# Kernel tuning notes

Measured on AMD Instinct MI355X. Metric: run time of the kernel, lower is better.

## Reference

```python
import jax, jax.numpy as jnp
import numpy as np

SEQ, B, IN, H, GATES = 2048, 64, 64, 128, 4 * 128


def setup_inputs() -> dict:
    key = jax.random.key(0)
    ks = jax.random.split(key, 12)
    s_in = 1.0 / np.sqrt(H)
    return {
        "data": jax.random.normal(ks[0], (SEQ, B, IN), dtype=jnp.float32),
        "Wih0": jax.random.normal(ks[1], (GATES, IN), dtype=jnp.float32) * s_in,
        "Whh0": jax.random.normal(ks[2], (GATES, H), dtype=jnp.float32) * s_in,
        "bih0": jax.random.normal(ks[3], (GATES,), dtype=jnp.float32) * s_in,
        "bhh0": jax.random.normal(ks[4], (GATES,), dtype=jnp.float32) * s_in,
        "Wih1": jax.random.normal(ks[5], (GATES, H), dtype=jnp.float32) * s_in,
        "Whh1": jax.random.normal(ks[6], (GATES, H), dtype=jnp.float32) * s_in,
        "bih1": jax.random.normal(ks[7], (GATES,), dtype=jnp.float32) * s_in,
        "bhh1": jax.random.normal(ks[8], (GATES,), dtype=jnp.float32) * s_in,
        "Wlin": jax.random.normal(ks[9], (1, H), dtype=jnp.float32) * s_in,
        "blin": jax.random.normal(ks[10], (1,), dtype=jnp.float32) * s_in,
    }


def _lstm_layer(x, Wih, Whh, bih, bhh):
    # x: [T, B, D_in]; torch gate order: i, f, g, o
    Bsz = x.shape[1]
    Hd = Whh.shape[1]
    b = bih + bhh
    # Precompute input projections for all timesteps in one big GEMM: [T, B, 4H]
    xproj = jnp.einsum('tbd,gd->tbg', x, Wih) + b

    def step(carry, xp_t):
        h, c = carry
        gates = xp_t + h @ Whh.T  # [B, 4H]
        i, f, g, o = jnp.split(gates, 4, axis=-1)
        i = jax.nn.sigmoid(i)
        f = jax.nn.sigmoid(f)
        g = jnp.tanh(g)
        o = jax.nn.sigmoid(o)
        c = f * c + i * g
        h = o * jnp.tanh(c)
        return (h, c), h

    h0 = jnp.zeros((Bsz, Hd), x.dtype)
    (_, _), ys = jax.lax.scan(step, (h0, h0), xproj)
    return ys  # [T, B, H]


def reference(data, Wih0, Whh0, bih0, bhh0, Wih1, Whh1, bih1, bhh1, Wlin, blin):
    h = _lstm_layer(data, Wih0, Whh0, bih0, bhh0)
    h = _lstm_layer(h, Wih1, Whh1, bih1, bhh1)
    vecs = h @ Wlin.T + blin  # [T, B, 1]
    # NOTE: original module computes tanh(vecs) but returns the pre-tanh vecs.
    return vecs
```

## Files before the change

kernel.cpp:

```cpp
#include <hip/hip_runtime.h>

#define SEQ_T 2048
#define BATCH 64

typedef _Float16 half2v __attribute__((ext_vector_type(2)));
typedef float floatx2 __attribute__((ext_vector_type(2)));

#if defined(__has_builtin)
#  if __has_builtin(__builtin_amdgcn_fdot2)
#    define HAVE_FDOT2 1
#  endif
#endif

__device__ __forceinline__ float fdot2f(half2v a, half2v b, float c) {
#ifdef HAVE_FDOT2
  return __builtin_amdgcn_fdot2(a, b, c, false);
#else
  return c + (float)a[0] * (float)b[0] + (float)a[1] * (float)b[1];
#endif
}

__device__ __forceinline__ floatx2 fma2(floatx2 a, floatx2 b, floatx2 c) {
#if __has_builtin(__builtin_elementwise_fma)
  return __builtin_elementwise_fma(a, b, c);
#else
  floatx2 r;
  r.x = __builtin_fmaf(a.x, b.x, c.x);
  r.y = __builtin_fmaf(a.y, b.y, c.y);
  return r;
#endif
}

__device__ __forceinline__ unsigned int h2u(half2v v) { return __builtin_bit_cast(unsigned int, v); }
__device__ __forceinline__ half2v u2h(unsigned int u) { return __builtin_bit_cast(half2v, u); }

template <int K, bool IN_F32>
__global__ __launch_bounds__(512) void xproj_gemm(
    const void* __restrict__ Xv,
    const float* __restrict__ W,
    const float* __restrict__ bih, const float* __restrict__ bhh,
    unsigned short* __restrict__ xp)
{
  constexpr int MT = 64;
  const int g = threadIdx.x;
  const size_t m0 = (size_t)blockIdx.x * MT;

  __shared__ __align__(16) _Float16 xs[MT * K];

  if constexpr (IN_F32) {
    constexpr int PER = MT * K / 512;
    const float* Xf = (const float*)Xv + m0 * K + (size_t)g * PER;
    _Float16* dst = xs + g * PER;
#pragma unroll
    for (int i = 0; i < PER; i += 4) {
      float4 v = *reinterpret_cast<const float4*>(Xf + i);
      half2v h01; h01[0] = (_Float16)v.x; h01[1] = (_Float16)v.y;
      half2v h23; h23[0] = (_Float16)v.z; h23[1] = (_Float16)v.w;
      uint2 u; u.x = h2u(h01); u.y = h2u(h23);
      *reinterpret_cast<uint2*>(dst + i) = u;
    }
  } else {
    constexpr int PER = MT * K / 512;
    const unsigned short* Xh = (const unsigned short*)Xv + m0 * K + (size_t)g * PER;
#pragma unroll
    for (int i = 0; i < PER / 8; i++)
      reinterpret_cast<uint4*>(xs + g * PER)[i] = reinterpret_cast<const uint4*>(Xh)[i];
  }

  half2v wr[K / 2];
  {
    const float2* p = reinterpret_cast<const float2*>(W + (size_t)g * K);
#pragma unroll
    for (int k = 0; k < K / 2; k++) {
      float2 f = p[k];
      half2v v; v[0] = (_Float16)f.x; v[1] = (_Float16)f.y;
      wr[k] = v;
    }
  }
  const float bias = bih[g] + bhh[g];
  const int out_off = (g & 127) * 4 + (g >> 7);
  __syncthreads();

#pragma unroll 1
  for (int tb = 0; tb < MT; tb++) {
    const uint4* xv = reinterpret_cast<const uint4*>(xs + tb * K);
    float a0 = bias, a1 = 0.f, a2 = 0.f, a3 = 0.f;
#pragma unroll
    for (int i = 0; i < K / 8; i++) {
      const uint4 u = xv[i];
      a0 = fdot2f(wr[4 * i + 0], u2h(u.x), a0);
      a1 = fdot2f(wr[4 * i + 1], u2h(u.y), a1);
      a2 = fdot2f(wr[4 * i + 2], u2h(u.z), a2);
      a3 = fdot2f(wr[4 * i + 3], u2h(u.w), a3);
    }
    const float s = (a0 + a1) + (a2 + a3);
    xp[(m0 + tb) * 512 + out_off] = __builtin_bit_cast(unsigned short, (_Float16)s);
  }
}

struct StepCtx {
  int ks, r, hidx;
  int li0, li1, li2, li3;
  float sc, am, ab;
  bool writer;
};

__device__ __forceinline__ float sigmoid_fast(float x) {
  return 1.f / (1.f + __expf(-x));
}

__device__ __forceinline__ void lstm_step(
    int cur, const StepCtx& cx,
    const floatx2 (&wh)[4][16], float (&hbuf)[2][144],
    unsigned short& pf, const unsigned short*& pf_ptr,
    float& c, unsigned short*& hout_ptr)
{
  const float xpv = (float)__builtin_bit_cast(_Float16, pf);
  pf = *pf_ptr;
  pf_ptr += 2 * BATCH * 512;

  floatx2 a0 = {0.f, 0.f}, a1 = {0.f, 0.f}, a2 = {0.f, 0.f}, a3 = {0.f, 0.f};
  const float4* hv = reinterpret_cast<const float4*>(&hbuf[cur][cx.ks * 36]);
#pragma unroll
  for (int i = 0; i < 8; i++) {
    const float4 u = hv[i];
    floatx2 lo; lo.x = u.x; lo.y = u.y;
    floatx2 hi; hi.x = u.z; hi.y = u.w;
    a0 = fma2(wh[0][2 * i], lo, a0); a0 = fma2(wh[0][2 * i + 1], hi, a0);
    a1 = fma2(wh[1][2 * i], lo, a1); a1 = fma2(wh[1][2 * i + 1], hi, a1);
    a2 = fma2(wh[2][2 * i], lo, a2); a2 = fma2(wh[2][2 * i + 1], hi, a2);
    a3 = fma2(wh[3][2 * i], lo, a3); a3 = fma2(wh[3][2 * i + 1], hi, a3);
  }
  float b0v = a0.x + a0.y;
  float b1v = a1.x + a1.y;
  float b2v = a2.x + a2.y;
  float b3v = a3.x + a3.y;

  const bool q0 = (cx.ks & 1) != 0, q1 = (cx.ks & 2) != 0;
  float s0 = q0 ? b0v : b1v;
  float s1 = q0 ? b2v : b3v;
  float r0 = __shfl_xor(s0, 1);
  float r1 = __shfl_xor(s1, 1);
  float kA = (q0 ? b1v : b0v) + r0;
  float kB = (q0 ? b3v : b2v) + r1;
  float s2 = q1 ? kA : kB;
  float r2 = __shfl_xor(s2, 2);
  float sum = (q1 ? kB : kA) + r2 + xpv;

  float y = cx.am * sigmoid_fast(cx.sc * sum) + cx.ab;

  float gi = __shfl(y, cx.li0);
  float gf = __shfl(y, cx.li1);
  float gg = __shfl(y, cx.li2);
  float go = __shfl(y, cx.li3);

  c = gf * c + gi * gg;
  float th = 2.f * sigmoid_fast(2.f * c) - 1.f;
  float h = go * th;

  if (cx.writer) {
    hbuf[cur ^ 1][cx.hidx] = h;
    *hout_ptr = __builtin_bit_cast(unsigned short, (_Float16)h);
  }
  hout_ptr += BATCH * 128;

  __syncthreads();
}

__global__ __launch_bounds__(512, 2) void lstm_rec2(
    const float* __restrict__ Whh,
    const unsigned short* __restrict__ xp,
    unsigned short* __restrict__ hout)
{
  const int b = blockIdx.x;
  const int tid = threadIdx.x;
  const int l = tid & 63;
  const int w = tid >> 6;
  const int rr = l >> 2;
  const int ks = l & 3;
  const int r = w * 16 + rr;

  __shared__ __align__(16) float hbuf[2][144];

  floatx2 wh[4][16];
#pragma unroll
  for (int g = 0; g < 4; g++) {
    const float4* p = reinterpret_cast<const float4*>(
        Whh + ((size_t)(g * 128 + r)) * 128 + ks * 32);
#pragma unroll
    for (int k = 0; k < 8; k++) {
      float4 f = p[k];
      floatx2 lo; lo.x = f.x; lo.y = f.y;
      floatx2 hi; hi.x = f.z; hi.y = f.w;
      wh[g][2 * k] = lo;
      wh[g][2 * k + 1] = hi;
    }
  }

  StepCtx cx;
  cx.ks = ks; cx.r = r;
  cx.hidx = (r >> 5) * 36 + (r & 31);
  const int lb = l & ~3;
  cx.li0 = lb + 0; cx.li1 = lb + 1; cx.li2 = lb + 2; cx.li3 = lb + 3;
  cx.sc = (ks == 2) ? 2.f : 1.f;
  cx.am = (ks == 2) ? 2.f : 1.f;
  cx.ab = (ks == 2) ? -1.f : 0.f;
  cx.writer = (ks == 0);

  if (tid < 144) { hbuf[0][tid] = 0.f; }

  const unsigned short* xpb = xp + (size_t)b * 512 + tid;
  unsigned short pfa = xpb[0];
  unsigned short pfb = xpb[(size_t)1 * (BATCH * 512)];
  const unsigned short* pA = xpb + (size_t)2 * (BATCH * 512);
  const unsigned short* pB = xpb + (size_t)3 * (BATCH * 512);
  unsigned short* houtp = hout + (size_t)b * 128 + r;
  float c = 0.f;
  __syncthreads();

#pragma unroll 1
  for (int t = 0; t < SEQ_T; t += 2) {
    lstm_step(0, cx, wh, hbuf, pfa, pA, c, houtp);
    lstm_step(1, cx, wh, hbuf, pfb, pB, c, houtp);
  }
}

__global__ __launch_bounds__(256) void final_lin(
    const unsigned short* __restrict__ h1,
    const float* __restrict__ Wlin, const float* __restrict__ blin,
    float* __restrict__ out)
{
  const size_t tb = (size_t)blockIdx.x * 256 + threadIdx.x;
  half2v wl[64];
  const float2* p = reinterpret_cast<const float2*>(Wlin);
#pragma unroll
  for (int k = 0; k < 64; k++) {
    float2 f = p[k];
    half2v v; v[0] = (_Float16)f.x; v[1] = (_Float16)f.y;
    wl[k] = v;
  }
  const uint4* hv = reinterpret_cast<const uint4*>(h1 + tb * 128);
  float a0 = 0.f, a1 = 0.f, a2 = 0.f, a3 = 0.f;
#pragma unroll
  for (int i = 0; i < 16; i++) {
    const uint4 u = hv[i];
    a0 = fdot2f(wl[4 * i + 0], u2h(u.x), a0);
    a1 = fdot2f(wl[4 * i + 1], u2h(u.y), a1);
    a2 = fdot2f(wl[4 * i + 2], u2h(u.z), a2);
    a3 = fdot2f(wl[4 * i + 3], u2h(u.w), a3);
  }
  out[tb] = (a0 + a1) + (a2 + a3) + blin[0];
}

extern "C" void kernel_launch(void* const* d_in, const int* in_sizes, int n_in,
                              void* d_out, int out_size, void* d_ws, size_t ws_size,
                              hipStream_t stream) {
  (void)in_sizes; (void)n_in; (void)out_size; (void)ws_size;

  const float* data = (const float*)d_in[0];
  const float* Wih0 = (const float*)d_in[1];
  const float* Whh0 = (const float*)d_in[2];
  const float* bih0 = (const float*)d_in[3];
  const float* bhh0 = (const float*)d_in[4];
  const float* Wih1 = (const float*)d_in[5];
  const float* Whh1 = (const float*)d_in[6];
  const float* bih1 = (const float*)d_in[7];
  const float* bhh1 = (const float*)d_in[8];
  const float* Wlin = (const float*)d_in[9];
  const float* blin = (const float*)d_in[10];

  unsigned char* ws = (unsigned char*)d_ws;
  unsigned short* xpb = (unsigned short*)ws;
  unsigned short* h0 = (unsigned short*)(ws + (size_t)128 * 1024 * 1024);
  unsigned short* h1 = (unsigned short*)(ws + (size_t)160 * 1024 * 1024);

  const int M = SEQ_T * BATCH;
  const int gemm_blocks = M / 64;

  xproj_gemm<64, true><<<dim3(gemm_blocks), dim3(512), 0, stream>>>(
      data, Wih0, bih0, bhh0, xpb);
  lstm_rec2<<<dim3(BATCH), dim3(512), 0, stream>>>(Whh0, xpb, h0);
  xproj_gemm<128, false><<<dim3(gemm_blocks), dim3(512), 0, stream>>>(
      h0, Wih1, bih1, bhh1, xpb);
  lstm_rec2<<<dim3(BATCH), dim3(512), 0, stream>>>(Whh1, xpb, h1);
  final_lin<<<dim3(M / 256), dim3(256), 0, stream>>>(h1, Wlin, blin, (float*)d_out);
}
```

Before: 3.195 ms.

## Split recurrent LSTM step over 1024 threads with DPP quad reductions

Moves the recurrent kernel from 512 threads, each reducing a 32-element K slice, to 1024 threads that each reduce a 16-element slice. This halves the serial dot-product work per thread on every step. Cross-lane shuffles (ds_bpermute) for the partial-sum reduction and gate broadcast are replaced with DPP quad permutes plus a half-row mirror, which should lower latency on the step's critical path. The cost is a 1024-thread barrier each step and twice as many redundant lanes computing gate activations.

```diff
diff --git a/kernel.cpp b/kernel.cpp
--- a/kernel.cpp
+++ b/kernel.cpp
@@ -33,6 +33,20 @@
 
 __device__ __forceinline__ unsigned int h2u(half2v v) { return __builtin_bit_cast(unsigned int, v); }
 __device__ __forceinline__ half2v u2h(unsigned int u) { return __builtin_bit_cast(half2v, u); }
+
+template <int CTRL>
+__device__ __forceinline__ float qperm(float x) {
+  int xi = __builtin_bit_cast(int, x);
+  int ri = __builtin_amdgcn_update_dpp(xi, xi, CTRL, 0xF, 0xF, true);
+  return __builtin_bit_cast(float, ri);
+}
+#define QP_XOR1   0xB1
+#define QP_XOR2   0x4E
+#define QP_B0     0x00
+#define QP_B1     0x55
+#define QP_B2     0xAA
+#define QP_B3     0xFF
+#define QP_HMIRR  0x141
 
 template <int K, bool IN_F32>
 __global__ __launch_bounds__(512) void xproj_gemm(
@@ -99,10 +113,9 @@
 }
 
 struct StepCtx {
-  int ks, r, hidx;
-  int li0, li1, li2, li3;
+  bool t0, t1, qsel, writer;
+  int hidx;
   float sc, am, ab;
-  bool writer;
 };
 
 __device__ __forceinline__ float sigmoid_fast(float x) {
@@ -111,7 +124,7 @@
 
 __device__ __forceinline__ void lstm_step(
     int cur, const StepCtx& cx,
-    const floatx2 (&wh)[4][16], float (&hbuf)[2][144],
+    const floatx2 (&wf)[4][8], float (&hbuf)[2][160], int o,
     unsigned short& pf, const unsigned short*& pf_ptr,
     float& c, unsigned short*& hout_ptr)
 {
@@ -119,44 +132,49 @@
   pf = *pf_ptr;
   pf_ptr += 2 * BATCH * 512;
 
-  floatx2 a0 = {0.f, 0.f}, a1 = {0.f, 0.f}, a2 = {0.f, 0.f}, a3 = {0.f, 0.f};
-  const float4* hv = reinterpret_cast<const float4*>(&hbuf[cur][cx.ks * 36]);
-#pragma unroll
-  for (int i = 0; i < 8; i++) {
+  const float4* hv = reinterpret_cast<const float4*>(&hbuf[cur][o * 20]);
+  floatx2 acc0 = {0.f, 0.f}, acc1 = {0.f, 0.f}, acc2 = {0.f, 0.f}, acc3 = {0.f, 0.f};
+#pragma unroll
+  for (int i = 0; i < 4; i++) {
     const float4 u = hv[i];
     floatx2 lo; lo.x = u.x; lo.y = u.y;
     floatx2 hi; hi.x = u.z; hi.y = u.w;
-    a0 = fma2(wh[0][2 * i], lo, a0); a0 = fma2(wh[0][2 * i + 1], hi, a0);
-    a1 = fma2(wh[1][2 * i], lo, a1); a1 = fma2(wh[1][2 * i + 1], hi, a1);
-    a2 = fma2(wh[2][2 * i], lo, a2); a2 = fma2(wh[2][2 * i + 1], hi, a2);
-    a3 = fma2(wh[3][2 * i], lo, a3); a3 = fma2(wh[3][2 * i + 1], hi, a3);
-  }
-  float b0v = a0.x + a0.y;
-  float b1v = a1.x + a1.y;
-  float b2v = a2.x + a2.y;
-  float b3v = a3.x + a3.y;
-
-  const bool q0 = (cx.ks & 1) != 0, q1 = (cx.ks & 2) != 0;
-  float s0 = q0 ? b0v : b1v;
-  float s1 = q0 ? b2v : b3v;
-  float r0 = __shfl_xor(s0, 1);
-  float r1 = __shfl_xor(s1, 1);
-  float kA = (q0 ? b1v : b0v) + r0;
-  float kB = (q0 ? b3v : b2v) + r1;
-  float s2 = q1 ? kA : kB;
-  float r2 = __shfl_xor(s2, 2);
-  float sum = (q1 ? kB : kA) + r2 + xpv;
-
-  float y = cx.am * sigmoid_fast(cx.sc * sum) + cx.ab;
-
-  float gi = __shfl(y, cx.li0);
-  float gf = __shfl(y, cx.li1);
-  float gg = __shfl(y, cx.li2);
-  float go = __shfl(y, cx.li3);
+    acc0 = fma2(wf[0][2 * i], lo, acc0); acc0 = fma2(wf[0][2 * i + 1], hi, acc0);
+    acc1 = fma2(wf[1][2 * i], lo, acc1); acc1 = fma2(wf[1][2 * i + 1], hi, acc1);
+    acc2 = fma2(wf[2][2 * i], lo, acc2); acc2 = fma2(wf[2][2 * i + 1], hi, acc2);
+    acc3 = fma2(wf[3][2 * i], lo, acc3); acc3 = fma2(wf[3][2 * i + 1], hi, acc3);
+  }
+  const float a0 = acc0.x + acc0.y;
+  const float a1 = acc1.x + acc1.y;
+  const float a2 = acc2.x + acc2.y;
+  const float a3 = acc3.x + acc3.y;
+
+  const float s0 = cx.t0 ? a0 : a1;
+  const float r0 = qperm<QP_XOR1>(s0);
+  const float kA = (cx.t0 ? a1 : a0) + r0;
+  const float s1 = cx.t0 ? a2 : a3;
+  const float r1 = qperm<QP_XOR1>(s1);
+  const float kB = (cx.t0 ? a3 : a2) + r1;
+  const float s2 = cx.t1 ? kA : kB;
+  const float r2 = qperm<QP_XOR2>(s2);
+  const float sq = (cx.t1 ? kB : kA) + r2;
+  const float sm = sq + qperm<QP_HMIRR>(sq);
+  const float sum = sm + xpv;
+
+  const float y = cx.am * sigmoid_fast(cx.sc * sum) + cx.ab;
+
+  const float b0v = qperm<QP_B0>(y);
+  const float b1v = qperm<QP_B1>(y);
+  const float b2v = qperm<QP_B2>(y);
+  const float b3v = qperm<QP_B3>(y);
+  const float gi = cx.qsel ? b3v : b0v;
+  const float gf = cx.qsel ? b2v : b1v;
+  const float gg = cx.qsel ? b1v : b2v;
+  const float go = cx.qsel ? b0v : b3v;
 
   c = gf * c + gi * gg;
-  float th = 2.f * sigmoid_fast(2.f * c) - 1.f;
-  float h = go * th;
+  const float th = 2.f * sigmoid_fast(2.f * c) - 1.f;
+  const float h = go * th;
 
   if (cx.writer) {
     hbuf[cur ^ 1][cx.hidx] = h;
@@ -167,49 +185,49 @@
   __syncthreads();
 }
 
-__global__ __launch_bounds__(512, 2) void lstm_rec2(
+__global__ __launch_bounds__(1024)
+__attribute__((amdgpu_waves_per_eu(4, 4)))
+void lstm_rec3(
     const float* __restrict__ Whh,
     const unsigned short* __restrict__ xp,
     unsigned short* __restrict__ hout)
 {
   const int b = blockIdx.x;
   const int tid = threadIdx.x;
-  const int l = tid & 63;
-  const int w = tid >> 6;
-  const int rr = l >> 2;
-  const int ks = l & 3;
-  const int r = w * 16 + rr;
-
-  __shared__ __align__(16) float hbuf[2][144];
-
-  floatx2 wh[4][16];
+  const int r = tid >> 3;
+  const int o = tid & 7;
+  const int m = (o < 4) ? o : (7 - o);
+
+  __shared__ __align__(16) float hbuf[2][160];
+
+  floatx2 wf[4][8];
 #pragma unroll
   for (int g = 0; g < 4; g++) {
     const float4* p = reinterpret_cast<const float4*>(
-        Whh + ((size_t)(g * 128 + r)) * 128 + ks * 32);
-#pragma unroll
-    for (int k = 0; k < 8; k++) {
+        Whh + ((size_t)(g * 128 + r)) * 128 + o * 16);
+#pragma unroll
+    for (int k = 0; k < 4; k++) {
       float4 f = p[k];
       floatx2 lo; lo.x = f.x; lo.y = f.y;
       floatx2 hi; hi.x = f.z; hi.y = f.w;
-      wh[g][2 * k] = lo;
-      wh[g][2 * k + 1] = hi;
+      wf[g][2 * k] = lo;
+      wf[g][2 * k + 1] = hi;
     }
   }
 
   StepCtx cx;
-  cx.ks = ks; cx.r = r;
-  cx.hidx = (r >> 5) * 36 + (r & 31);
-  const int lb = l & ~3;
-  cx.li0 = lb + 0; cx.li1 = lb + 1; cx.li2 = lb + 2; cx.li3 = lb + 3;
-  cx.sc = (ks == 2) ? 2.f : 1.f;
-  cx.am = (ks == 2) ? 2.f : 1.f;
-  cx.ab = (ks == 2) ? -1.f : 0.f;
-  cx.writer = (ks == 0);
-
-  if (tid < 144) { hbuf[0][tid] = 0.f; }
-
-  const unsigned short* xpb = xp + (size_t)b * 512 + tid;
+  cx.t0 = (m & 1) != 0;
+  cx.t1 = (m & 2) != 0;
+  cx.qsel = (o >= 4);
+  cx.writer = (o == 0);
+  cx.hidx = (r >> 4) * 20 + (r & 15);
+  cx.sc = (m == 2) ? 2.f : 1.f;
+  cx.am = (m == 2) ? 2.f : 1.f;
+  cx.ab = (m == 2) ? -1.f : 0.f;
+
+  if (tid < 160) hbuf[0][tid] = 0.f;
+
+  const unsigned short* xpb = xp + (size_t)b * 512 + (r * 4 + m);
   unsigned short pfa = xpb[0];
   unsigned short pfb = xpb[(size_t)1 * (BATCH * 512)];
   const unsigned short* pA = xpb + (size_t)2 * (BATCH * 512);
@@ -220,8 +238,8 @@
 
 #pragma unroll 1
   for (int t = 0; t < SEQ_T; t += 2) {
-    lstm_step(0, cx, wh, hbuf, pfa, pA, c, houtp);
-    lstm_step(1, cx, wh, hbuf, pfb, pB, c, houtp);
+    lstm_step(0, cx, wf, hbuf, o, pfa, pA, c, houtp);
+    lstm_step(1, cx, wf, hbuf, o, pfb, pB, c, houtp);
   }
 }
 
@@ -279,9 +297,9 @@
 
   xproj_gemm<64, true><<<dim3(gemm_blocks), dim3(512), 0, stream>>>(
       data, Wih0, bih0, bhh0, xpb);
-  lstm_rec2<<<dim3(BATCH), dim3(512), 0, stream>>>(Whh0, xpb, h0);
+  lstm_rec3<<<dim3(BATCH), dim3(1024), 0, stream>>>(Whh0, xpb, h0);
   xproj_gemm<128, false><<<dim3(gemm_blocks), dim3(512), 0, stream>>>(
       h0, Wih1, bih1, bhh1, xpb);
-  lstm_rec2<<<dim3(BATCH), dim3(512), 0, stream>>>(Whh1, xpb, h1);
+  lstm_rec3<<<dim3(BATCH), dim3(1024), 0, stream>>>(Whh1, xpb, h1);
   final_lin<<<dim3(M / 256), dim3(256), 0, stream>>>(h1, Wlin, blin, (float*)d_out);
 }
```

After: 3.783 ms. +18.4%, slower.
